# Performance work log

Hardware: AMD Instinct MI355X
Metric: run time of the kernel (lower is better)

Reference implementation:

```python
import jax, jax.numpy as jnp
import numpy as np

N_NODES = 50000
N_EDGES = 800000
IN_CH = 128
HID = 256
NUM_LAYERS = 3


def setup_inputs() -> dict:
    key = jax.random.key(0)
    ks = jax.random.split(key, 16)
    x = jax.random.normal(ks[0], (N_NODES, IN_CH), dtype=jnp.float32)
    edge_index = jax.random.randint(ks[1], (2, N_EDGES), 0, N_NODES, dtype=jnp.int64)
    inp = {"x": x, "edge_index": edge_index}
    dims = [(IN_CH, HID), (HID, HID), (HID, HID)]
    for i, (din, dout) in enumerate(dims):
        s = 1.0 / np.sqrt(din)
        # lin_l (applied to aggregated neighbors, has bias), lin_r (root, no bias)
        inp[f"Wl{i}"] = jax.random.uniform(ks[2 + 3 * i], (din, dout), jnp.float32, -s, s)
        inp[f"b{i}"] = jax.random.uniform(ks[3 + 3 * i], (dout,), jnp.float32, -s, s)
        inp[f"Wr{i}"] = jax.random.uniform(ks[4 + 3 * i], (din, dout), jnp.float32, -s, s)
    return inp


def _sage_layer(x, src, dst, Wl, b, Wr):
    # mean aggregation of source-node features at destination nodes
    msg = x[src]  # [E, din]
    summed = jax.ops.segment_sum(msg, dst, num_segments=N_NODES)
    cnt = jax.ops.segment_sum(jnp.ones((src.shape[0], 1), x.dtype), dst, num_segments=N_NODES)
    agg = summed / jnp.maximum(cnt, 1.0)
    return agg @ Wl + b + x @ Wr


def reference(x, edge_index, Wl0, b0, Wr0, Wl1, b1, Wr1, Wl2, b2, Wr2):
    src, dst = edge_index[0], edge_index[1]
    params = [(Wl0, b0, Wr0), (Wl1, b1, Wr1), (Wl2, b2, Wr2)]
    h = x
    for i, (Wl, b, Wr) in enumerate(params):
        h = _sage_layer(h, src, dst, Wl, b, Wr)
        if i < NUM_LAYERS - 1:
            h = jax.nn.relu(h)  # dropout p=0.0 -> identity
    return h
```

## Files before the change

kernel.cpp:

```cpp
#include <hip/hip_runtime.h>
#include <hip/hip_bf16.h>

#define N_NODES 50000
#define N_EDGES 800000
#define MBLKS ((N_NODES + 255) / 256)
#define XCD_RANGE 6250
#define SLOT_CAP 64
#define EDGE_GROUP_BLOCKS 200
#define GBLOCKS 800

typedef __attribute__((ext_vector_type(4))) float f32x4;
typedef __attribute__((ext_vector_type(16))) float f32x16;
typedef __attribute__((ext_vector_type(8))) short s16x8;

__device__ int   g_cursor[N_NODES];
__device__ __attribute__((aligned(256))) int g_adjf[(size_t)N_NODES * SLOT_CAP];
__device__ __attribute__((aligned(256))) unsigned short g_aggbf[(size_t)N_NODES * 256];
__device__ __attribute__((aligned(256))) unsigned short g_bf0[(size_t)N_NODES * 256];
__device__ __attribute__((aligned(256))) unsigned short g_bf1[(size_t)N_NODES * 256];
__device__ __attribute__((aligned(256))) unsigned short g_Whi[6][256 * 256];

__device__ __forceinline__ unsigned short f2bf(float f) {
    unsigned int u = __float_as_uint(f);
    unsigned int r = (u + 0x7fffu + ((u >> 16) & 1u)) >> 16;
    return (unsigned short)r;
}
__device__ __forceinline__ float bf2f(unsigned short h) {
    return __uint_as_float(((unsigned int)h) << 16);
}

__global__ void zero_kernel() {
    int i = blockIdx.x * blockDim.x + threadIdx.x;
    if (i < N_NODES) g_cursor[i] = 0;
}

__device__ __forceinline__ void prep_w_seg(const float* __restrict__ W, int K,
                                           int widx, int lbx, int tid) {
    int e = lbx * 256 + tid;
    if (e >= K * 256) return;
    int k = e >> 8, n = e & 255;
    g_Whi[widx][n * K + k] = f2bf(W[e]);
}

__global__ void build_prep_kernel(const int* __restrict__ ei, const float* __restrict__ x,
                                  const float* __restrict__ Wl0, const float* __restrict__ Wr0,
                                  const float* __restrict__ Wl1, const float* __restrict__ Wr1,
                                  const float* __restrict__ Wl2, const float* __restrict__ Wr2) {
    int bx = blockIdx.x;
    int tid = threadIdx.x;
    if (bx < 8 * EDGE_GROUP_BLOCKS) {
        const int grp = bx & 7;
        const int gbx = bx >> 3;
        const int lo = grp * XCD_RANGE, hi = lo + XCD_RANGE;
        const int NQ = N_EDGES / 4;
        for (int q = gbx * 256 + tid; q < NQ; q += EDGE_GROUP_BLOCKS * 256) {
            int4 s4 = *(const int4*)(ei + q * 4);
            int4 d4 = *(const int4*)(ei + N_EDGES + q * 4);
            if (d4.x >= lo && d4.x < hi) {
                int p = atomicAdd(&g_cursor[d4.x], 1);
                if (p < SLOT_CAP) g_adjf[(long)d4.x * SLOT_CAP + p] = ((unsigned)s4.x < N_NODES) ? s4.x : 0;
            }
            if (d4.y >= lo && d4.y < hi) {
                int p = atomicAdd(&g_cursor[d4.y], 1);
                if (p < SLOT_CAP) g_adjf[(long)d4.y * SLOT_CAP + p] = ((unsigned)s4.y < N_NODES) ? s4.y : 0;
            }
            if (d4.z >= lo && d4.z < hi) {
                int p = atomicAdd(&g_cursor[d4.z], 1);
                if (p < SLOT_CAP) g_adjf[(long)d4.z * SLOT_CAP + p] = ((unsigned)s4.z < N_NODES) ? s4.z : 0;
            }
            if (d4.w >= lo && d4.w < hi) {
                int p = atomicAdd(&g_cursor[d4.w], 1);
                if (p < SLOT_CAP) g_adjf[(long)d4.w * SLOT_CAP + p] = ((unsigned)s4.w < N_NODES) ? s4.w : 0;
            }
        }
        return;
    }
    bx -= 8 * EDGE_GROUP_BLOCKS;
    if (bx < 128)   { prep_w_seg(Wl0, 128, 0, bx, tid);        return; }
    if (bx < 256)   { prep_w_seg(Wr0, 128, 1, bx - 128, tid);  return; }
    if (bx < 512)   { prep_w_seg(Wl1, 256, 2, bx - 256, tid);  return; }
    if (bx < 768)   { prep_w_seg(Wr1, 256, 3, bx - 512, tid);  return; }
    if (bx < 1024)  { prep_w_seg(Wl2, 256, 4, bx - 768, tid);  return; }
    if (bx < 1280)  { prep_w_seg(Wr2, 256, 5, bx - 1024, tid); return; }
    long i = (long)(bx - 1280) * 256 + tid;
    if (i >= (long)N_NODES * 128 / 8) return;
    const float* xp = x + i * 8;
    f32x4 v0 = *(const f32x4*)(xp);
    f32x4 v1 = *(const f32x4*)(xp + 4);
    s16x8 o;
    o[0] = (short)f2bf(v0.x); o[1] = (short)f2bf(v0.y);
    o[2] = (short)f2bf(v0.z); o[3] = (short)f2bf(v0.w);
    o[4] = (short)f2bf(v1.x); o[5] = (short)f2bf(v1.y);
    o[6] = (short)f2bf(v1.z); o[7] = (short)f2bf(v1.w);
    *(s16x8*)(g_bf0 + i * 8) = o;
}

template <int DIN>
__global__ __launch_bounds__(256) void agg_wave_kernel(int sel) {
    const unsigned short* __restrict__ hb = sel == 0 ? g_bf0 : g_bf1;
    constexpr int LPR = DIN / 8;
    constexpr int RPW = 64 / LPR;
    const int node = blockIdx.x * 4 + (threadIdx.x >> 6);
    if (node >= N_NODES) return;
    const int lane = threadIdx.x & 63;
    const int rg = lane / LPR;
    const int cl = lane % LPR;
    const int cnt = g_cursor[node];
    const int e = (cnt < SLOT_CAP) ? cnt : SLOT_CAP;
    const int* __restrict__ adj = g_adjf + (long)node * SLOT_CAP;

    float acc[8];
#pragma unroll
    for (int j = 0; j < 8; ++j) acc[j] = 0.f;

    int i = 0;
    for (; i + 8 * RPW <= e; i += 8 * RPW) {
        int a[8];
#pragma unroll
        for (int u = 0; u < 8; ++u) a[u] = adj[i + u * RPW + rg];
        s16x8 v[8];
#pragma unroll
        for (int u = 0; u < 8; ++u) v[u] = *(const s16x8*)(hb + (long)a[u] * DIN + cl * 8);
#pragma unroll
        for (int u = 0; u < 8; ++u)
#pragma unroll
            for (int j = 0; j < 8; ++j) acc[j] += bf2f((unsigned short)v[u][j]);
    }
    for (; i + 4 * RPW <= e; i += 4 * RPW) {
        int a[4];
#pragma unroll
        for (int u = 0; u < 4; ++u) a[u] = adj[i + u * RPW + rg];
        s16x8 v[4];
#pragma unroll
        for (int u = 0; u < 4; ++u) v[u] = *(const s16x8*)(hb + (long)a[u] * DIN + cl * 8);
#pragma unroll
        for (int u = 0; u < 4; ++u)
#pragma unroll
            for (int j = 0; j < 8; ++j) acc[j] += bf2f((unsigned short)v[u][j]);
    }
    for (; i < e; i += RPW) {
        int eidx = i + rg;
        if (eidx < e) {
            int a = adj[eidx];
            s16x8 v = *(const s16x8*)(hb + (long)a * DIN + cl * 8);
#pragma unroll
            for (int j = 0; j < 8; ++j) acc[j] += bf2f((unsigned short)v[j]);
        }
    }

#pragma unroll
    for (int j = 0; j < 8; ++j) {
        if (RPW == 4) acc[j] += __shfl_xor(acc[j], 16, 64);
        acc[j] += __shfl_xor(acc[j], 32, 64);
    }

    if (rg == 0) {
        float inv = 1.f / fmaxf((float)cnt, 1.f);
        s16x8 ov;
#pragma unroll
        for (int j = 0; j < 8; ++j) ov[j] = (short)f2bf(acc[j] * inv);
        *(s16x8*)(g_aggbf + (long)node * DIN + cl * 8) = ov;
    }
}

template <int K, bool RELU, bool FP32OUT>
__global__ __launch_bounds__(256, 4) void gemm2_mfma(
    int a2_sel, int widx, const float* __restrict__ bias,
    float* __restrict__ outp, int bfsel) {
    __shared__ __attribute__((aligned(16))) char lds[40960];
    char* const As = lds;
    char* const Wh = lds + 32768;

    const int tid = threadIdx.x;
    const int w = tid >> 6;
    const int l = tid & 63;
    const int l31 = l & 31;
    const int lh = l >> 5;
    const int bx = blockIdx.x;
    const int xcd = bx & 7;
    const int idx = bx >> 3;
    const int mblk = (idx >> 2) * 8 + xcd;
    const int nblk = idx & 3;
    if (mblk >= MBLKS) return;
    const long row0 = (long)mblk * 256;
    const int ncol0 = nblk * 64;

    f32x16 acc[2][2];
#pragma unroll
    for (int i = 0; i < 2; ++i)
#pragma unroll
        for (int j = 0; j < 2; ++j) acc[i][j] = (f32x16)0.f;

    const int sar = tid >> 3;
    const int sac = tid & 7;
    const int swn = tid >> 2;
    const int swc = (tid & 3) * 2;

    const unsigned short* A2p = a2_sel == 0 ? (const unsigned short*)g_bf0
                                            : (const unsigned short*)g_bf1;
    constexpr int NPP = K / 64;
    constexpr int NT = NPP * 2;

    s16x8 aR[8], whR[2];
    auto issue = [&](int t) {
        int pass = (t >= NPP) ? 1 : 0;
        int kc = (t - pass * NPP) * 64;
        const unsigned short* A = pass ? A2p : (const unsigned short*)g_aggbf;
        const unsigned short* WH = g_Whi[widx + pass] + (long)ncol0 * K;
#pragma unroll
        for (int j = 0; j < 8; ++j) {
            int r = j * 32 + sar;
            long grow = row0 + r; if (grow > N_NODES - 1) grow = N_NODES - 1;
            aR[j] = *(const s16x8*)(A + grow * K + kc + sac * 8);
        }
#pragma unroll
        for (int q = 0; q < 2; ++q) {
            int c = swc + q;
            whR[q] = *(const s16x8*)(WH + (long)swn * K + kc + c * 8);
        }
    };

    issue(0);
    for (int t = 0; t < NT; ++t) {
#pragma unroll
        for (int j = 0; j < 8; ++j) {
            int r = j * 32 + sar;
            *(s16x8*)(As + r * 128 + ((sac * 16) ^ ((r & 7) << 4))) = aR[j];
        }
#pragma unroll
        for (int q = 0; q < 2; ++q) {
            int c = swc + q;
            int o = swn * 128 + ((c * 16) ^ ((swn & 7) << 4));
            *(s16x8*)(Wh + o) = whR[q];
        }
        __syncthreads();
        if (t + 1 < NT) issue(t + 1);
#pragma unroll
        for (int ks = 0; ks < 4; ++ks) {
            const int kb = ks * 32 + lh * 16;
            s16x8 af[2], bh[2];
#pragma unroll
            for (int mi = 0; mi < 2; ++mi) {
                int r = w * 64 + mi * 32 + l31;
                af[mi] = *(const s16x8*)(As + r * 128 + (kb ^ ((r & 7) << 4)));
            }
#pragma unroll
            for (int ni = 0; ni < 2; ++ni) {
                int n = ni * 32 + l31;
                int o = n * 128 + (kb ^ ((n & 7) << 4));
                bh[ni] = *(const s16x8*)(Wh + o);
            }
#pragma unroll
            for (int mi = 0; mi < 2; ++mi)
#pragma unroll
                for (int ni = 0; ni < 2; ++ni)
                    acc[mi][ni] = __builtin_amdgcn_mfma_f32_32x32x16_bf16(af[mi], bh[ni], acc[mi][ni], 0, 0, 0);
        }
        __syncthreads();
    }

    unsigned short* bfout = bfsel == 0 ? g_bf0 : g_bf1;
#pragma unroll
    for (int ni = 0; ni < 2; ++ni) {
        int col = ncol0 + ni * 32 + l31;
        float bv = bias[col];
#pragma unroll
        for (int mi = 0; mi < 2; ++mi) {
#pragma unroll
            for (int reg = 0; reg < 16; ++reg) {
                int lr = (reg & 3) + 8 * (reg >> 2) + 4 * lh;
                long grow = row0 + w * 64 + mi * 32 + lr;
                if (grow < N_NODES) {
                    float v = acc[mi][ni][reg] + bv;
                    if (RELU) v = fmaxf(v, 0.f);
                    if (FP32OUT) outp[grow * 256 + col] = v;
                    else bfout[grow * 256 + col] = f2bf(v);
                }
            }
        }
    }
}

extern "C" void kernel_launch(void* const* d_in, const int* in_sizes, int n_in,
                              void* d_out, int out_size, void* d_ws, size_t ws_size,
                              hipStream_t stream) {
    const float* x = (const float*)d_in[0];
    const int* ei = (const int*)d_in[1];
    const float* Wl0 = (const float*)d_in[2];
    const float* b0  = (const float*)d_in[3];
    const float* Wr0 = (const float*)d_in[4];
    const float* Wl1 = (const float*)d_in[5];
    const float* b1  = (const float*)d_in[6];
    const float* Wr1 = (const float*)d_in[7];
    const float* Wl2 = (const float*)d_in[8];
    const float* b2  = (const float*)d_in[9];
    const float* Wr2 = (const float*)d_in[10];
    float* out = (float*)d_out;

    int nblocks = (N_NODES + 255) / 256;
    int ablocks = (N_NODES + 3) / 4;

    zero_kernel<<<nblocks, 256, 0, stream>>>();
    build_prep_kernel<<<8 * EDGE_GROUP_BLOCKS + 1280 + 3125, 256, 0, stream>>>(
        ei, x, Wl0, Wr0, Wl1, Wr1, Wl2, Wr2);

    agg_wave_kernel<128><<<ablocks, 256, 0, stream>>>(0);
    gemm2_mfma<128, true, false><<<GBLOCKS, 256, 0, stream>>>(0, 0, b0, nullptr, 1);

    agg_wave_kernel<256><<<ablocks, 256, 0, stream>>>(1);
    gemm2_mfma<256, true, false><<<GBLOCKS, 256, 0, stream>>>(1, 2, b1, nullptr, 0);

    agg_wave_kernel<256><<<ablocks, 256, 0, stream>>>(0);
    gemm2_mfma<256, false, true><<<GBLOCKS, 256, 0, stream>>>(0, 4, b2, out, 1);
}
```

Measured before the change: 328.9 us.

## Use 8-wave GEMM blocks and grid-stride persistent aggregation

```diff
diff --git a/kernel.cpp b/kernel.cpp
--- a/kernel.cpp
+++ b/kernel.cpp
@@ -8,6 +8,7 @@
 #define SLOT_CAP 64
 #define EDGE_GROUP_BLOCKS 200
 #define GBLOCKS 800
+#define AGG_BLOCKS 3125
 
 typedef __attribute__((ext_vector_type(4))) float f32x4;
 typedef __attribute__((ext_vector_type(16))) float f32x16;
@@ -100,71 +101,73 @@
     const unsigned short* __restrict__ hb = sel == 0 ? g_bf0 : g_bf1;
     constexpr int LPR = DIN / 8;
     constexpr int RPW = 64 / LPR;
-    const int node = blockIdx.x * 4 + (threadIdx.x >> 6);
-    if (node >= N_NODES) return;
     const int lane = threadIdx.x & 63;
     const int rg = lane / LPR;
     const int cl = lane % LPR;
-    const int cnt = g_cursor[node];
-    const int e = (cnt < SLOT_CAP) ? cnt : SLOT_CAP;
-    const int* __restrict__ adj = g_adjf + (long)node * SLOT_CAP;
-
-    float acc[8];
-#pragma unroll
-    for (int j = 0; j < 8; ++j) acc[j] = 0.f;
-
-    int i = 0;
-    for (; i + 8 * RPW <= e; i += 8 * RPW) {
-        int a[8];
-#pragma unroll
-        for (int u = 0; u < 8; ++u) a[u] = adj[i + u * RPW + rg];
-        s16x8 v[8];
-#pragma unroll
-        for (int u = 0; u < 8; ++u) v[u] = *(const s16x8*)(hb + (long)a[u] * DIN + cl * 8);
-#pragma unroll
-        for (int u = 0; u < 8; ++u)
-#pragma unroll
-            for (int j = 0; j < 8; ++j) acc[j] += bf2f((unsigned short)v[u][j]);
-    }
-    for (; i + 4 * RPW <= e; i += 4 * RPW) {
-        int a[4];
-#pragma unroll
-        for (int u = 0; u < 4; ++u) a[u] = adj[i + u * RPW + rg];
-        s16x8 v[4];
-#pragma unroll
-        for (int u = 0; u < 4; ++u) v[u] = *(const s16x8*)(hb + (long)a[u] * DIN + cl * 8);
-#pragma unroll
-        for (int u = 0; u < 4; ++u)
-#pragma unroll
-            for (int j = 0; j < 8; ++j) acc[j] += bf2f((unsigned short)v[u][j]);
-    }
-    for (; i < e; i += RPW) {
-        int eidx = i + rg;
-        if (eidx < e) {
-            int a = adj[eidx];
-            s16x8 v = *(const s16x8*)(hb + (long)a * DIN + cl * 8);
-#pragma unroll
-            for (int j = 0; j < 8; ++j) acc[j] += bf2f((unsigned short)v[j]);
-        }
-    }
-
-#pragma unroll
-    for (int j = 0; j < 8; ++j) {
-        if (RPW == 4) acc[j] += __shfl_xor(acc[j], 16, 64);
-        acc[j] += __shfl_xor(acc[j], 32, 64);
-    }
-
-    if (rg == 0) {
-        float inv = 1.f / fmaxf((float)cnt, 1.f);
-        s16x8 ov;
-#pragma unroll
-        for (int j = 0; j < 8; ++j) ov[j] = (short)f2bf(acc[j] * inv);
-        *(s16x8*)(g_aggbf + (long)node * DIN + cl * 8) = ov;
+    const int wave0 = blockIdx.x * 4 + (threadIdx.x >> 6);
+
+    for (int node = wave0; node < N_NODES; node += AGG_BLOCKS * 4) {
+        const int cnt = g_cursor[node];
+        const int e = (cnt < SLOT_CAP) ? cnt : SLOT_CAP;
+        const int* __restrict__ adj = g_adjf + (long)node * SLOT_CAP;
+
+        float acc[8];
+#pragma unroll
+        for (int j = 0; j < 8; ++j) acc[j] = 0.f;
+
+        int i = 0;
+        for (; i + 8 * RPW <= e; i += 8 * RPW) {
+            int a[8];
+#pragma unroll
+            for (int u = 0; u < 8; ++u) a[u] = adj[i + u * RPW + rg];
+            s16x8 v[8];
+#pragma unroll
+            for (int u = 0; u < 8; ++u) v[u] = *(const s16x8*)(hb + (long)a[u] * DIN + cl * 8);
+#pragma unroll
+            for (int u = 0; u < 8; ++u)
+#pragma unroll
+                for (int j = 0; j < 8; ++j) acc[j] += bf2f((unsigned short)v[u][j]);
+        }
+        for (; i + 4 * RPW <= e; i += 4 * RPW) {
+            int a[4];
+#pragma unroll
+            for (int u = 0; u < 4; ++u) a[u] = adj[i + u * RPW + rg];
+            s16x8 v[4];
+#pragma unroll
+            for (int u = 0; u < 4; ++u) v[u] = *(const s16x8*)(hb + (long)a[u] * DIN + cl * 8);
+#pragma unroll
+            for (int u = 0; u < 4; ++u)
+#pragma unroll
+                for (int j = 0; j < 8; ++j) acc[j] += bf2f((unsigned short)v[u][j]);
+        }
+        for (; i < e; i += RPW) {
+            int eidx = i + rg;
+            if (eidx < e) {
+                int a = adj[eidx];
+                s16x8 v = *(const s16x8*)(hb + (long)a * DIN + cl * 8);
+#pragma unroll
+                for (int j = 0; j < 8; ++j) acc[j] += bf2f((unsigned short)v[j]);
+            }
+        }
+
+#pragma unroll
+        for (int j = 0; j < 8; ++j) {
+            if (RPW == 4) acc[j] += __shfl_xor(acc[j], 16, 64);
+            acc[j] += __shfl_xor(acc[j], 32, 64);
+        }
+
+        if (rg == 0) {
+            float inv = 1.f / fmaxf((float)cnt, 1.f);
+            s16x8 ov;
+#pragma unroll
+            for (int j = 0; j < 8; ++j) ov[j] = (short)f2bf(acc[j] * inv);
+            *(s16x8*)(g_aggbf + (long)node * DIN + cl * 8) = ov;
+        }
     }
 }
 
 template <int K, bool RELU, bool FP32OUT>
-__global__ __launch_bounds__(256, 4) void gemm2_mfma(
+__global__ __launch_bounds__(512, 6) void gemm2_mfma(
     int a2_sel, int widx, const float* __restrict__ bias,
     float* __restrict__ outp, int bfsel) {
     __shared__ __attribute__((aligned(16))) char lds[40960];
@@ -185,76 +188,57 @@
     const long row0 = (long)mblk * 256;
     const int ncol0 = nblk * 64;
 
-    f32x16 acc[2][2];
-#pragma unroll
-    for (int i = 0; i < 2; ++i)
-#pragma unroll
-        for (int j = 0; j < 2; ++j) acc[i][j] = (f32x16)0.f;
+    f32x16 acc[2];
+    acc[0] = (f32x16)0.f;
+    acc[1] = (f32x16)0.f;
 
     const int sar = tid >> 3;
     const int sac = tid & 7;
-    const int swn = tid >> 2;
-    const int swc = (tid & 3) * 2;
+    const int swn = tid >> 3;
 
     const unsigned short* A2p = a2_sel == 0 ? (const unsigned short*)g_bf0
                                             : (const unsigned short*)g_bf1;
     constexpr int NPP = K / 64;
     constexpr int NT = NPP * 2;
 
-    s16x8 aR[8], whR[2];
+    s16x8 aR[4], whR;
     auto issue = [&](int t) {
         int pass = (t >= NPP) ? 1 : 0;
         int kc = (t - pass * NPP) * 64;
         const unsigned short* A = pass ? A2p : (const unsigned short*)g_aggbf;
         const unsigned short* WH = g_Whi[widx + pass] + (long)ncol0 * K;
 #pragma unroll
-        for (int j = 0; j < 8; ++j) {
-            int r = j * 32 + sar;
+        for (int j = 0; j < 4; ++j) {
+            int r = j * 64 + sar;
             long grow = row0 + r; if (grow > N_NODES - 1) grow = N_NODES - 1;
             aR[j] = *(const s16x8*)(A + grow * K + kc + sac * 8);
         }
-#pragma unroll
-        for (int q = 0; q < 2; ++q) {
-            int c = swc + q;
-            whR[q] = *(const s16x8*)(WH + (long)swn * K + kc + c * 8);
-        }
+        whR = *(const s16x8*)(WH + (long)swn * K + kc + sac * 8);
     };
 
     issue(0);
     for (int t = 0; t < NT; ++t) {
 #pragma unroll
-        for (int j = 0; j < 8; ++j) {
-            int r = j * 32 + sar;
+        for (int j = 0; j < 4; ++j) {
+            int r = j * 64 + sar;
             *(s16x8*)(As + r * 128 + ((sac * 16) ^ ((r & 7) << 4))) = aR[j];
         }
-#pragma unroll
-        for (int q = 0; q < 2; ++q) {
-            int c = swc + q;
-            int o = swn * 128 + ((c * 16) ^ ((swn & 7) << 4));
-            *(s16x8*)(Wh + o) = whR[q];
-        }
+        *(s16x8*)(Wh + swn * 128 + ((sac * 16) ^ ((swn & 7) << 4))) = whR;
         __syncthreads();
         if (t + 1 < NT) issue(t + 1);
 #pragma unroll
         for (int ks = 0; ks < 4; ++ks) {
             const int kb = ks * 32 + lh * 16;
-            s16x8 af[2], bh[2];
-#pragma unroll
-            for (int mi = 0; mi < 2; ++mi) {
-                int r = w * 64 + mi * 32 + l31;
-                af[mi] = *(const s16x8*)(As + r * 128 + (kb ^ ((r & 7) << 4)));
-            }
+            int r = w * 32 + l31;
+            s16x8 af = *(const s16x8*)(As + r * 128 + (kb ^ ((r & 7) << 4)));
+            s16x8 bh[2];
 #pragma unroll
             for (int ni = 0; ni < 2; ++ni) {
                 int n = ni * 32 + l31;
-                int o = n * 128 + (kb ^ ((n & 7) << 4));
-                bh[ni] = *(const s16x8*)(Wh + o);
-            }
-#pragma unroll
-            for (int mi = 0; mi < 2; ++mi)
-#pragma unroll
-                for (int ni = 0; ni < 2; ++ni)
-                    acc[mi][ni] = __builtin_amdgcn_mfma_f32_32x32x16_bf16(af[mi], bh[ni], acc[mi][ni], 0, 0, 0);
+                bh[ni] = *(const s16x8*)(Wh + n * 128 + (kb ^ ((n & 7) << 4)));
+            }
+            acc[0] = __builtin_amdgcn_mfma_f32_32x32x16_bf16(af, bh[0], acc[0], 0, 0, 0);
+            acc[1] = __builtin_amdgcn_mfma_f32_32x32x16_bf16(af, bh[1], acc[1], 0, 0, 0);
         }
         __syncthreads();
     }
@@ -265,17 +249,14 @@
         int col = ncol0 + ni * 32 + l31;
         float bv = bias[col];
 #pragma unroll
-        for (int mi = 0; mi < 2; ++mi) {
-#pragma unroll
-            for (int reg = 0; reg < 16; ++reg) {
-                int lr = (reg & 3) + 8 * (reg >> 2) + 4 * lh;
-                long grow = row0 + w * 64 + mi * 32 + lr;
-                if (grow < N_NODES) {
-                    float v = acc[mi][ni][reg] + bv;
-                    if (RELU) v = fmaxf(v, 0.f);
-                    if (FP32OUT) outp[grow * 256 + col] = v;
-                    else bfout[grow * 256 + col] = f2bf(v);
-                }
+        for (int reg = 0; reg < 16; ++reg) {
+            int lr = (reg & 3) + 8 * (reg >> 2) + 4 * lh;
+            long grow = row0 + w * 32 + lr;
+            if (grow < N_NODES) {
+                float v = acc[ni][reg] + bv;
+                if (RELU) v = fmaxf(v, 0.f);
+                if (FP32OUT) outp[grow * 256 + col] = v;
+                else bfout[grow * 256 + col] = f2bf(v);
             }
         }
     }
@@ -298,18 +279,17 @@
     float* out = (float*)d_out;
 
     int nblocks = (N_NODES + 255) / 256;
-    int ablocks = (N_NODES + 3) / 4;
 
     zero_kernel<<<nblocks, 256, 0, stream>>>();
     build_prep_kernel<<<8 * EDGE_GROUP_BLOCKS + 1280 + 3125, 256, 0, stream>>>(
         ei, x, Wl0, Wr0, Wl1, Wr1, Wl2, Wr2);
 
-    agg_wave_kernel<128><<<ablocks, 256, 0, stream>>>(0);
-    gemm2_mfma<128, true, false><<<GBLOCKS, 256, 0, stream>>>(0, 0, b0, nullptr, 1);
-
-    agg_wave_kernel<256><<<ablocks, 256, 0, stream>>>(1);
-    gemm2_mfma<256, true, false><<<GBLOCKS, 256, 0, stream>>>(1, 2, b1, nullptr, 0);
-
-    agg_wave_kernel<256><<<ablocks, 256, 0, stream>>>(0);
-    gemm2_mfma<256, false, true><<<GBLOCKS, 256, 0, stream>>>(0, 4, b2, out, 1);
-}
+    agg_wave_kernel<128><<<AGG_BLOCKS, 256, 0, stream>>>(0);
+    gemm2_mfma<128, true, false><<<GBLOCKS, 512, 0, stream>>>(0, 0, b0, nullptr, 1);
+
+    agg_wave_kernel<256><<<AGG_BLOCKS, 256, 0, stream>>>(1);
+    gemm2_mfma<256, true, false><<<GBLOCKS, 512, 0, stream>>>(1, 2, b1, nullptr, 0);
+
+    agg_wave_kernel<256><<<AGG_BLOCKS, 256, 0, stream>>>(0);
+    gemm2_mfma<256, false, true><<<GBLOCKS, 512, 0, stream>>>(0, 4, b2, out, 1);
+}
```

Result: faster. 293.1 us (-10.9%).
